# Performance work log

Hardware: AMD Instinct MI355X
Metric: run time of the kernel (lower is better)

Reference implementation:

```python
import jax, jax.numpy as jnp
import numpy as np

B, T, E, H = 4, 2048, 1024, 2048  # note: T must equal H (mask shape constraint in source)


def setup_inputs() -> dict:
    key = jax.random.key(0)
    ks = jax.random.split(key, 5)
    x = jax.random.normal(ks[0], (B, T, E), dtype=jnp.float32)
    Wq = jax.random.normal(ks[1], (E, H), dtype=jnp.float32) * 0.02
    bq = jnp.zeros((H,), dtype=jnp.float32)
    Wv = jax.random.normal(ks[2], (E, H), dtype=jnp.float32) * 0.02
    bv = jnp.zeros((H,), dtype=jnp.float32)
    return {"x": x, "Wq": Wq, "bq": bq, "Wv": Wv, "bv": bv}


def reference(x, Wq, bq, Wv, bv):
    # NOTE: original code uses q_proj for BOTH q and k (k = self.q_proj(x)),
    # so k is identical to q; k_proj params are dead. We reproduce that.
    q = x @ Wq + bq                                  # [B, T, H]
    v = x @ Wv + bv                                  # [B, T, H]
    scores = jnp.einsum('bqd,bkd->bqk', q, q)        # q @ k.mT with k == q
    scaled = scores / jnp.sqrt(jnp.float32(Wq.shape[1]))
    mask = jnp.tril(jnp.ones((scaled.shape[1], scaled.shape[2]), dtype=scaled.dtype))
    masked = scaled * mask                           # multiplicative mask (as in source)
    attn = jax.nn.softmax(masked, axis=1)            # softmax over dim=1 (query axis), as in source
    return attn @ v                                  # [B, T, H]
```

## Files before the change

### kernel.cpp

```cpp
#include <hip/hip_runtime.h>


#define B_DIM 4
#define T_DIM 2048
#define E_DIM 1024
#define H_DIM 2048

typedef __attribute__((ext_vector_type(8))) short bf16x8;
typedef __attribute__((ext_vector_type(4))) short s16x4;
typedef __attribute__((ext_vector_type(4))) float f32x4;

__device__ __forceinline__ float bf2f(short s) {
  union { float f; unsigned u; } x; x.u = ((unsigned)(unsigned short)s) << 16; return x.f;
}
__device__ __forceinline__ short f2bf(float f) {
  union { float f; unsigned u; } x; x.f = f;
  unsigned r = x.u + 0x7fff + ((x.u >> 16) & 1);
  return (short)(r >> 16);
}

__device__ __forceinline__ void gload16(const short* g, short* l) {
  __builtin_amdgcn_global_load_lds(
      (const __attribute__((address_space(1))) void*)g,
      (__attribute__((address_space(3))) void*)l, 16, 0, 0);
}

template<int MODE>
__global__ __launch_bounds__(512, 2) void gemm256(
    const short* __restrict__ Ag, const short* __restrict__ Bg,
    const float* __restrict__ bias, const float* __restrict__ bias2,
    void* __restrict__ Cg, void* __restrict__ Cg2,
    const float* __restrict__ sfx,
    int N, int K, long sA, long sB, long sC)
{
  __shared__ __align__(16) short lds[4 * 16384];

  const int t = threadIdx.x;
  const int lane = t & 63, wave = t >> 6;
  const int wm = wave >> 2, wn = wave & 3;
  const int l16 = lane & 15, kg = lane >> 4;

  int rt, ct, bz;
  if (MODE == 2) { rt = blockIdx.x; ct = blockIdx.y; bz = blockIdx.z; }
  else           { rt = blockIdx.y; ct = blockIdx.x; bz = 0; }

  const short* A  = Ag + (long)bz * sA + (long)rt * 256 * K;
  const short* Bp = Bg + (long)bz * sB + (long)ct * 256 * K;
  const int kEnd = (MODE == 2) ? (rt + 1) * 256 : K;
  const int NT = kEnd >> 5;

  const int sr = t >> 2;
  const int scg = (t & 3) ^ ((sr >> 2) & 3);
  const long a0 = (long)sr * K + scg * 8;
  const long a1 = a0 + 128L * K;

  const int swz = kg ^ ((l16 >> 2) & 3);
  const int aoff = (wm * 128 + l16) * 32 + swz * 8;
  const int boff = (wn * 64 + l16) * 32 + swz * 8;

  f32x4 acc[8][4] = {};

#pragma unroll
  for (int s = 0; s < 3; ++s) {
    short* L = &lds[s * 16384];
    const long k0 = (long)s * 32;
    gload16(A + a0 + k0, L + t * 8);
    gload16(A + a1 + k0, L + 4096 + t * 8);
    gload16(Bp + a0 + k0, L + 8192 + t * 8);
    gload16(Bp + a1 + k0, L + 12288 + t * 8);
  }
  asm volatile("s_waitcnt vmcnt(8)" ::: "memory");
  __builtin_amdgcn_s_barrier();

  for (int ts = 0; ts < NT; ++ts) {
    const short* Ab = &lds[(ts & 3) * 16384];
    const short* Bb = Ab + 8192;
    short* Ls = &lds[((ts + 3) & 3) * 16384];
    const long k3 = (long)(ts + 3) * 32;
    const bool st = (ts + 3) < NT;

    bf16x8 bfrag[4], afrag[4];
#pragma unroll
    for (int n = 0; n < 4; ++n) bfrag[n] = *(const bf16x8*)&Bb[boff + n * 512];
#pragma unroll
    for (int m = 0; m < 4; ++m) afrag[m] = *(const bf16x8*)&Ab[aoff + m * 512];
    if (st) {
      gload16(A + a0 + k3, Ls + t * 8);
      gload16(A + a1 + k3, Ls + 4096 + t * 8);
    }
    __builtin_amdgcn_s_barrier();
    __builtin_amdgcn_s_setprio(1);
#pragma unroll
    for (int m = 0; m < 4; ++m)
#pragma unroll
      for (int n = 0; n < 4; ++n)
        acc[m][n] = __builtin_amdgcn_mfma_f32_16x16x32_bf16(afrag[m], bfrag[n], acc[m][n], 0, 0, 0);
    __builtin_amdgcn_s_setprio(0);
    __builtin_amdgcn_s_barrier();
#pragma unroll
    for (int m = 0; m < 4; ++m) afrag[m] = *(const bf16x8*)&Ab[aoff + (m + 4) * 512];
    if (st) {
      gload16(Bp + a0 + k3, Ls + 8192 + t * 8);
      gload16(Bp + a1 + k3, Ls + 12288 + t * 8);
    }
    __builtin_amdgcn_s_barrier();
    __builtin_amdgcn_s_setprio(1);
#pragma unroll
    for (int m = 0; m < 4; ++m)
#pragma unroll
      for (int n = 0; n < 4; ++n)
        acc[m + 4][n] = __builtin_amdgcn_mfma_f32_16x16x32_bf16(afrag[m], bfrag[n], acc[m + 4][n], 0, 0, 0);
    __builtin_amdgcn_s_setprio(0);
    asm volatile("s_waitcnt lgkmcnt(0)" ::: "memory");
    const int w = NT - 2 - ts;
    if (w >= 2)      asm volatile("s_waitcnt vmcnt(8)" ::: "memory");
    else if (w == 1) asm volatile("s_waitcnt vmcnt(4)" ::: "memory");
    else if (w == 0) asm volatile("s_waitcnt vmcnt(0)" ::: "memory");
    __builtin_amdgcn_s_barrier();
  }

  __syncthreads();

  if (MODE == 0) {
    short* Cs = lds;
    const int Nh = N >> 1;
#pragma unroll
    for (int m = 0; m < 8; ++m)
#pragma unroll
      for (int n = 0; n < 4; ++n) {
        const int cl = wn * 64 + n * 16 + l16;
        const int colg = ct * 256 + cl;
        const float bv = (colg < Nh) ? bias[colg] : bias2[colg - Nh];
#pragma unroll
        for (int r = 0; r < 4; ++r) {
          const int rl = wm * 128 + m * 16 + kg * 4 + r;
          *(short*)((char*)Cs + (((((rl << 8) + cl) << 1)) ^ ((rl & 7) << 4))) =
              f2bf(acc[m][n][r] + bv);
        }
      }
    __syncthreads();
    short* C = ((ct * 256) < Nh) ? (short*)Cg : (short*)Cg2;
    const int rr = t >> 1, hc = (t & 1) * 128;
    const long gbase = (long)(rt * 256 + rr) * Nh + ((ct * 256) & (Nh - 1)) + hc;
#pragma unroll
    for (int j = 0; j < 16; ++j)
      *(bf16x8*)(C + gbase + j * 8) =
          *(const bf16x8*)((const char*)Cs +
              ((((rr << 8) + hc + (j << 3)) << 1) ^ ((rr & 7) << 4)));
  } else {
    float* C = (float*)Cg + (long)bz * sC;
    const float* sf = sfx + ((long)bz * 16 + 2 * rt + 1) * N;
    const int rowb = rt * 256 + wm * 128 + kg * 4;
    const int colb = ct * 256 + wn * 64 + l16;
#pragma unroll
    for (int m = 0; m < 8; ++m)
#pragma unroll
      for (int n = 0; n < 4; ++n) {
        const int col = colb + n * 16;
        const float s = sf[col];
#pragma unroll
        for (int r = 0; r < 4; ++r)
          C[(long)(rowb + m * 16 + r) * N + col] = acc[m][n][r] + s;
      }
  }
}

template<int MODE>
__global__ __launch_bounds__(256) void gemm_bt(
    const short* __restrict__ Ag, const short* __restrict__ Bg,
    const float* __restrict__ bias, const float* __restrict__ bias2,
    void* __restrict__ Cg, void* __restrict__ Cg2,
    float* __restrict__ colsum, const float* __restrict__ sfx,
    int M, int N, int K, long sA, long sB, long sC, float scale)
{
  __shared__ __align__(16) short lds[128 * 64 * 2];
  short* As = lds;
  short* Bs = lds + 128 * 64;
  __shared__ float csum[128];

  const int t = threadIdx.x;
  const int bz = blockIdx.z;

  int rt, ct;
  if (MODE == 1) {
    int idx = 135 - blockIdx.x;
    rt = (int)((sqrtf(8.0f * idx + 1.0f) - 1.0f) * 0.5f);
    while ((rt + 1) * (rt + 2) / 2 <= idx) rt++;
    while (rt * (rt + 1) / 2 > idx) rt--;
    ct = idx - rt * (rt + 1) / 2;
  } else if (MODE == 2) {
    rt = (gridDim.x - 1) - blockIdx.x;
    ct = blockIdx.y;
  } else {
    rt = blockIdx.y; ct = blockIdx.x;
  }

  const short* A = Ag + (long)bz * sA + (long)rt * 128 * K;
  const short* B = Bg + (long)bz * sB + (long)ct * 128 * K;
  const int kEnd = (MODE == 2) ? (rt + 1) * 128 : K;

  const int lane = t & 63;
  const int wave = t >> 6;
  const int wr = wave >> 1, wc = wave & 1;
  const int l16 = lane & 15, kg = lane >> 4;

  if (MODE == 1) { if (t < 128) csum[t] = (rt == ct) ? 128.0f * ct : 0.0f; }

  f32x4 acc[4][4] = {};

  for (int k0 = 0; k0 < kEnd; k0 += 64) {
    __syncthreads();
#pragma unroll
    for (int j = 0; j < 4; ++j) {
      const int e = j * 256 + t;
      const int r = e >> 3, cl = e & 7;
      const int cg = cl ^ (r & 7);
      gload16(A + (long)r * K + (k0 + cg * 8), &As[e * 8]);
      gload16(B + (long)r * K + (k0 + cg * 8), &Bs[e * 8]);
    }
    __syncthreads();
#pragma unroll
    for (int kk = 0; kk < 2; ++kk) {
      bf16x8 af[4], bfr[4];
#pragma unroll
      for (int mi = 0; mi < 4; ++mi)
        af[mi] = *(const bf16x8*)&As[(wr * 64 + mi * 16 + l16) * 64 +
                                     ((kk * 4 + kg) ^ (l16 & 7)) * 8];
#pragma unroll
      for (int ni = 0; ni < 4; ++ni)
        bfr[ni] = *(const bf16x8*)&Bs[(wc * 64 + ni * 16 + l16) * 64 +
                                      ((kk * 4 + kg) ^ (l16 & 7)) * 8];
#pragma unroll
      for (int mi = 0; mi < 4; ++mi)
#pragma unroll
        for (int ni = 0; ni < 4; ++ni)
          acc[mi][ni] = __builtin_amdgcn_mfma_f32_16x16x32_bf16(af[mi], bfr[ni], acc[mi][ni], 0, 0, 0);
    }
  }

  if (MODE == 1) {
    short* Cs = lds;
    __syncthreads();
    float ps[4] = {0.f, 0.f, 0.f, 0.f};
#pragma unroll
    for (int mi = 0; mi < 4; ++mi)
#pragma unroll
      for (int ni = 0; ni < 4; ++ni) {
        const int cl = wc * 64 + ni * 16 + l16;
        const int col = ct * 128 + cl;
#pragma unroll
        for (int r = 0; r < 4; ++r) {
          const int rl = wr * 64 + kg * 4 + mi * 16 + r;
          const int row = rt * 128 + rl;
          float e = (row >= col) ? __expf(acc[mi][ni][r] * scale) : 1.0f;
          Cs[rl * 128 + cl] = f2bf(e);
          ps[ni] += e;
        }
      }
#pragma unroll
    for (int ni = 0; ni < 4; ++ni)
      atomicAdd(&csum[wc * 64 + ni * 16 + l16], ps[ni]);
    __syncthreads();
    short* C = (short*)Cg + (long)bz * sC;
    const int rr = t >> 1, cc = (t & 1) * 64;
    const long gbase = (long)(rt * 128 + rr) * N + ct * 128 + cc;
#pragma unroll
    for (int j = 0; j < 8; ++j)
      *(bf16x8*)(C + gbase + j * 8) = *(const bf16x8*)&Cs[rr * 128 + cc + j * 8];
    if (t < 128)
      atomicAdd(&colsum[(long)bz * N + ct * 128 + t], csum[t]);
  } else if (MODE == 0) {
    short* Cs = lds;
    __syncthreads();
    const int Nh = N >> 1;
#pragma unroll
    for (int mi = 0; mi < 4; ++mi)
#pragma unroll
      for (int ni = 0; ni < 4; ++ni) {
        const int cl = wc * 64 + ni * 16 + l16;
        const int colg = ct * 128 + cl;
        const float bv = (colg < Nh) ? bias[colg] : bias2[colg - Nh];
#pragma unroll
        for (int r = 0; r < 4; ++r) {
          const int rl = wr * 64 + kg * 4 + mi * 16 + r;
          Cs[rl * 128 + cl] = f2bf(acc[mi][ni][r] + bv);
        }
      }
    __syncthreads();
    short* C = (ct * 128 < Nh) ? (short*)Cg : (short*)Cg2;
    const int colofs = (ct * 128) & (Nh - 1);
    const int rr = t >> 1, cc = (t & 1) * 64;
    const long gbase = (long)(rt * 128 + rr) * Nh + colofs + cc;
#pragma unroll
    for (int j = 0; j < 8; ++j)
      *(bf16x8*)(C + gbase + j * 8) = *(const bf16x8*)&Cs[rr * 128 + cc + j * 8];
  } else {
    const int rowb = rt * 128 + wr * 64 + kg * 4;
    const int colb = ct * 128 + wc * 64 + l16;
    float* C = (float*)Cg + (long)bz * sC;
    const float* sf = sfx + ((long)bz * 16 + rt) * N;
#pragma unroll
    for (int mi = 0; mi < 4; ++mi)
#pragma unroll
      for (int ni = 0; ni < 4; ++ni) {
        int col = colb + ni * 16;
        float s = sf[col];
#pragma unroll
        for (int r = 0; r < 4; ++r) {
          int row = rowb + mi * 16 + r;
          C[(long)row * N + col] = acc[mi][ni][r] + s;
        }
      }
  }
}

__global__ __launch_bounds__(256) void ones_fill(short* __restrict__ P)
{
  const int r = blockIdx.x, bz = blockIdx.z;
  short* p = P + (long)bz * T_DIM * T_DIM +
             (long)(2 * r) * 128 * T_DIM + (2 * r + 1) * 128;
  const int t = threadIdx.x;
  const int row = t >> 1, c0 = (t & 1) * 64;
  bf16x8 ones;
#pragma unroll
  for (int j = 0; j < 8; ++j) ones[j] = (short)0x3F80;
#pragma unroll
  for (int j = 0; j < 8; ++j)
    *(bf16x8*)(p + (long)row * T_DIM + c0 + j * 8) = ones;
}

__global__ __launch_bounds__(256) void f32_to_bf16(
    const float* __restrict__ src, short* __restrict__ dst, long n)
{
  long i = ((long)blockIdx.x * blockDim.x + threadIdx.x) * 4;
  if (i < n) {
    const float4 v = *(const float4*)(src + i);
    s16x4 o;
    o.x = f2bf(v.x); o.y = f2bf(v.y); o.z = f2bf(v.z); o.w = f2bf(v.w);
    *(s16x4*)(dst + i) = o;
  }
}

__global__ __launch_bounds__(256) void wtrans(
    const float* __restrict__ src0, const float* __restrict__ src1,
    short* __restrict__ dst)
{
  __shared__ short tile[64][65];
  const int t = threadIdx.x;
  const int c0 = blockIdx.x * 64;
  const int r0 = blockIdx.y * 64;
  const float* s = blockIdx.z ? src1 : src0;
  short* d = dst + (long)blockIdx.z * H_DIM * E_DIM;
  const int rl = t >> 4, cb = (t & 15) * 4;
#pragma unroll
  for (int i = 0; i < 4; ++i) {
    int r = rl + i * 16;
    const float4 w = *(const float4*)(s + (long)(r0 + r) * H_DIM + c0 + cb);
    tile[r][cb + 0] = f2bf(w.x); tile[r][cb + 1] = f2bf(w.y);
    tile[r][cb + 2] = f2bf(w.z); tile[r][cb + 3] = f2bf(w.w);
  }
  __syncthreads();
#pragma unroll
  for (int i = 0; i < 4; ++i) {
    int rr = rl + i * 16;
    s16x4 o;
    o.x = tile[cb + 0][rr]; o.y = tile[cb + 1][rr];
    o.z = tile[cb + 2][rr]; o.w = tile[cb + 3][rr];
    *(s16x4*)(d + (long)(c0 + rr) * E_DIM + r0 + cb) = o;
  }
}

__global__ __launch_bounds__(256) void vtrans(
    const short* __restrict__ src, short* __restrict__ dst,
    const float* __restrict__ sums)
{
  __shared__ short tile[64][65];
  const int t = threadIdx.x;
  const int c0 = blockIdx.x * 64;
  const int r0 = blockIdx.y * 64;
  const int bz = blockIdx.z;
  const short* s = src + (long)bz * T_DIM * H_DIM;
  short* d = dst + (long)bz * H_DIM * T_DIM;
  const float* su = sums + (long)bz * T_DIM;
  const int rl = t >> 4, cb = (t & 15) * 4;
#pragma unroll
  for (int i = 0; i < 4; ++i) {
    int r = rl + i * 16;
    const float rs = 1.0f / su[r0 + r];
    const s16x4 w = *(const s16x4*)(s + (long)(r0 + r) * H_DIM + c0 + cb);
    tile[r][cb + 0] = f2bf(bf2f(w.x) * rs); tile[r][cb + 1] = f2bf(bf2f(w.y) * rs);
    tile[r][cb + 2] = f2bf(bf2f(w.z) * rs); tile[r][cb + 3] = f2bf(bf2f(w.w) * rs);
  }
  __syncthreads();
#pragma unroll
  for (int i = 0; i < 4; ++i) {
    int rr = rl + i * 16;
    s16x4 o;
    o.x = tile[cb + 0][rr]; o.y = tile[cb + 1][rr];
    o.z = tile[cb + 2][rr]; o.w = tile[cb + 3][rr];
    *(s16x4*)(d + (long)(c0 + rr) * T_DIM + r0 + cb) = o;
  }
}

__global__ __launch_bounds__(256) void block_psum(
    const short* __restrict__ v, const float* __restrict__ colsum,
    float* __restrict__ psum)
{
  const int h = (blockIdx.x * 256 + threadIdx.x) * 2;
  const int j = blockIdx.y, bz = blockIdx.z;
  const short* vb = v + (long)bz * T_DIM * H_DIM;
  const float* cs = colsum + (long)bz * T_DIM;
  float s0 = 0.f, s1 = 0.f;
  const int k0 = j * 128;
  for (int k = k0; k < k0 + 128; ++k) {
    union { int i; short s[2]; } w;
    w.i = *(const int*)(vb + (long)k * H_DIM + h);
    const float rs = 1.0f / cs[k];
    s0 += bf2f(w.s[0]) * rs;
    s1 += bf2f(w.s[1]) * rs;
  }
  float* p = psum + ((long)bz * 16 + j) * H_DIM + h;
  p[0] = s0; p[1] = s1;
}

__global__ __launch_bounds__(256) void suffix_scan(
    const float* __restrict__ psum, float* __restrict__ sfx)
{
  const int h = blockIdx.x * 256 + threadIdx.x;
  const int bz = blockIdx.z;
  const long base = (long)bz * 16 * H_DIM + h;
  float suf = 0.f;
  sfx[base + 15L * H_DIM] = 0.f;
  for (int j = 15; j >= 1; --j) {
    suf += psum[base + (long)j * H_DIM];
    sfx[base + (long)(j - 1) * H_DIM] = suf;
  }
}

extern "C" void kernel_launch(void* const* d_in, const int* in_sizes, int n_in,
                              void* d_out, int out_size, void* d_ws, size_t ws_size,
                              hipStream_t stream) {
  const float* x  = (const float*)d_in[0];
  const float* Wq = (const float*)d_in[1];
  const float* bq = (const float*)d_in[2];
  const float* Wv = (const float*)d_in[3];
  const float* bv = (const float*)d_in[4];
  float* out = (float*)d_out;

  char* ws = (char*)d_ws;
  short* P      = (short*)(ws);
  short* q      = (short*)(ws + (size_t)32 * 1024 * 1024);
  short* v      = (short*)(ws + (size_t)64 * 1024 * 1024);
  float* colsum = (float*)(ws + (size_t)96 * 1024 * 1024);
  float* sfx    = (float*)(ws + (size_t)96 * 1024 * 1024 + 32 * 1024);
  short* vT = q;

  short* xb    = (short*)d_out;
  short* WqvT  = (short*)((char*)d_out + (size_t)16 * 1024 * 1024);
  float* psum  = (float*)((char*)d_out + (size_t)24 * 1024 * 1024);

  const float scale = 0.022097086912079612f;
  dim3 blk(256);

  hipMemsetAsync(colsum, 0, (size_t)B_DIM * T_DIM * 4, stream);

  f32_to_bf16<<<dim3((B_DIM * T_DIM * E_DIM) / (256 * 4)), blk, 0, stream>>>(
      x, xb, (long)B_DIM * T_DIM * E_DIM);
  wtrans<<<dim3(H_DIM / 64, E_DIM / 64, 2), blk, 0, stream>>>(Wq, Wv, WqvT);

  gemm256<0><<<dim3((2 * H_DIM) / 256, (B_DIM * T_DIM) / 256, 1), dim3(512), 0, stream>>>(
      xb, WqvT, bq, bv, q, v, nullptr, 2 * H_DIM, E_DIM, 0, 0, 0);

  gemm_bt<1><<<dim3(136, 1, B_DIM), blk, 0, stream>>>(
      q, q, nullptr, nullptr, P, nullptr, colsum, nullptr, T_DIM, T_DIM, H_DIM,
      (long)T_DIM * H_DIM, (long)T_DIM * H_DIM, (long)T_DIM * T_DIM, scale);

  ones_fill<<<dim3(8, 1, B_DIM), blk, 0, stream>>>(P);

  vtrans<<<dim3(H_DIM / 64, T_DIM / 64, B_DIM), blk, 0, stream>>>(v, vT, colsum);
  block_psum<<<dim3(H_DIM / 512, 16, B_DIM), blk, 0, stream>>>(v, colsum, psum);
  suffix_scan<<<dim3(H_DIM / 256, 1, B_DIM), blk, 0, stream>>>(psum, sfx);

  gemm256<2><<<dim3(T_DIM / 256, H_DIM / 256, B_DIM), dim3(512), 0, stream>>>(
      P, vT, nullptr, nullptr, out, nullptr, sfx, H_DIM, T_DIM,
      (long)T_DIM * T_DIM, (long)H_DIM * T_DIM, (long)T_DIM * H_DIM);
}
```

Measured before the change: 359.3 us.

## Use 64-deep K double-buffered LDS pipeline and XCD-aware block remap in gemm256

Restructures the 256x256 GEMM main loop from a 4-stage ring of 32-wide K slices to a double-buffered scheme with 64-wide K tiles, each split into two halves, using a new paired-row swizzled LDS layout. This halves loop iterations and barrier overhead per K element. For non-batched modes it also remaps linear block IDs so consecutive tiles land on the same XCD, aiming for better L2 reuse. Unused MODE 0/2 paths in the 128-tile kernel are removed. Prefetch depth drops from three stages to one, which may expose more global-load latency.

```diff
diff --git a/kernel.cpp b/kernel.cpp
--- a/kernel.cpp
+++ b/kernel.cpp
@@ -33,7 +33,7 @@
     const float* __restrict__ sfx,
     int N, int K, long sA, long sB, long sC)
 {
-  __shared__ __align__(16) short lds[4 * 16384];
+  __shared__ __align__(16) short lds[2 * 32768];
 
   const int t = threadIdx.x;
   const int lane = t & 63, wave = t >> 6;
@@ -42,81 +42,138 @@
 
   int rt, ct, bz;
   if (MODE == 2) { rt = blockIdx.x; ct = blockIdx.y; bz = blockIdx.z; }
-  else           { rt = blockIdx.y; ct = blockIdx.x; bz = 0; }
+  else {
+    int lin = blockIdx.y * gridDim.x + blockIdx.x;
+    const int cpx = (gridDim.x * gridDim.y) >> 3;
+    lin = (lin & 7) * cpx + (lin >> 3);
+    rt = lin / gridDim.x; ct = lin - rt * gridDim.x;
+    bz = 0;
+  }
 
   const short* A  = Ag + (long)bz * sA + (long)rt * 256 * K;
   const short* Bp = Bg + (long)bz * sB + (long)ct * 256 * K;
   const int kEnd = (MODE == 2) ? (rt + 1) * 256 : K;
-  const int NT = kEnd >> 5;
-
-  const int sr = t >> 2;
-  const int scg = (t & 3) ^ ((sr >> 2) & 3);
-  const long a0 = (long)sr * K + scg * 8;
-  const long a1 = a0 + 128L * K;
-
-  const int swz = kg ^ ((l16 >> 2) & 3);
-  const int aoff = (wm * 128 + l16) * 32 + swz * 8;
-  const int boff = (wn * 64 + l16) * 32 + swz * 8;
+  const int NT = kEnd >> 6;
+
+  long soff[2];
+  int dsto[2];
+#pragma unroll
+  for (int j = 0; j < 2; ++j) {
+    const int cid = j * 512 + t;
+    const int f = cid >> 3, sl = cid & 7;
+    const int c = sl ^ (f & 7);
+    soff[j] = (long)(2 * f + (c >> 2)) * K + (c & 3) * 8;
+    dsto[j] = cid * 8;
+  }
+
+  const int fl = l16 >> 1;
+  const int slot = (((l16 & 1) * 4 + kg) ^ fl) & 7;
+  const int aoff = (wm * 64 + fl) * 64 + slot * 8;
+  const int boff = (wn * 32 + fl) * 64 + slot * 8;
 
   f32x4 acc[8][4] = {};
 
-#pragma unroll
-  for (int s = 0; s < 3; ++s) {
-    short* L = &lds[s * 16384];
-    const long k0 = (long)s * 32;
-    gload16(A + a0 + k0, L + t * 8);
-    gload16(A + a1 + k0, L + 4096 + t * 8);
-    gload16(Bp + a0 + k0, L + 8192 + t * 8);
-    gload16(Bp + a1 + k0, L + 12288 + t * 8);
-  }
-  asm volatile("s_waitcnt vmcnt(8)" ::: "memory");
-  __builtin_amdgcn_s_barrier();
-
-  for (int ts = 0; ts < NT; ++ts) {
-    const short* Ab = &lds[(ts & 3) * 16384];
-    const short* Bb = Ab + 8192;
-    short* Ls = &lds[((ts + 3) & 3) * 16384];
-    const long k3 = (long)(ts + 3) * 32;
-    const bool st = (ts + 3) < NT;
-
-    bf16x8 bfrag[4], afrag[4];
-#pragma unroll
-    for (int n = 0; n < 4; ++n) bfrag[n] = *(const bf16x8*)&Bb[boff + n * 512];
-#pragma unroll
-    for (int m = 0; m < 4; ++m) afrag[m] = *(const bf16x8*)&Ab[aoff + m * 512];
-    if (st) {
-      gload16(A + a0 + k3, Ls + t * 8);
-      gload16(A + a1 + k3, Ls + 4096 + t * 8);
-    }
-    __builtin_amdgcn_s_barrier();
-    __builtin_amdgcn_s_setprio(1);
-#pragma unroll
-    for (int m = 0; m < 4; ++m)
-#pragma unroll
-      for (int n = 0; n < 4; ++n)
-        acc[m][n] = __builtin_amdgcn_mfma_f32_16x16x32_bf16(afrag[m], bfrag[n], acc[m][n], 0, 0, 0);
-    __builtin_amdgcn_s_setprio(0);
-    __builtin_amdgcn_s_barrier();
-#pragma unroll
-    for (int m = 0; m < 4; ++m) afrag[m] = *(const bf16x8*)&Ab[aoff + (m + 4) * 512];
-    if (st) {
-      gload16(Bp + a0 + k3, Ls + 8192 + t * 8);
-      gload16(Bp + a1 + k3, Ls + 12288 + t * 8);
-    }
-    __builtin_amdgcn_s_barrier();
-    __builtin_amdgcn_s_setprio(1);
-#pragma unroll
-    for (int m = 0; m < 4; ++m)
-#pragma unroll
-      for (int n = 0; n < 4; ++n)
-        acc[m + 4][n] = __builtin_amdgcn_mfma_f32_16x16x32_bf16(afrag[m], bfrag[n], acc[m + 4][n], 0, 0, 0);
-    __builtin_amdgcn_s_setprio(0);
-    asm volatile("s_waitcnt lgkmcnt(0)" ::: "memory");
-    const int w = NT - 2 - ts;
-    if (w >= 2)      asm volatile("s_waitcnt vmcnt(8)" ::: "memory");
-    else if (w == 1) asm volatile("s_waitcnt vmcnt(4)" ::: "memory");
-    else if (w == 0) asm volatile("s_waitcnt vmcnt(0)" ::: "memory");
-    __builtin_amdgcn_s_barrier();
+  {
+    short* S = lds;
+#pragma unroll
+    for (int kh = 0; kh < 2; ++kh)
+#pragma unroll
+      for (int j = 0; j < 2; ++j) {
+        gload16(A  + soff[j] + kh * 32, &S[kh * 8192 + dsto[j]]);
+        gload16(Bp + soff[j] + kh * 32, &S[16384 + kh * 8192 + dsto[j]]);
+      }
+  }
+  asm volatile("s_waitcnt vmcnt(4)" ::: "memory");
+  asm volatile("s_barrier" ::: "memory");
+
+  for (int T = 0; T < NT; ++T) {
+    const short* Abase = lds + (T & 1) * 32768;
+    short* S = lds + ((T + 1) & 1) * 32768;
+    const long kIss = (long)(T + 1) * 64;
+    const bool st = (T + 1) < NT;
+    bf16x8 bfr[4], af[4];
+
+    {
+      const short* Ab = Abase;
+      const short* Bb = Abase + 16384;
+#pragma unroll
+      for (int n = 0; n < 4; ++n) bfr[n] = *(const bf16x8*)&Bb[boff + n * 512];
+#pragma unroll
+      for (int m = 0; m < 4; ++m) af[m] = *(const bf16x8*)&Ab[aoff + m * 512];
+      if (st) {
+        gload16(A + soff[0] + kIss, &S[dsto[0]]);
+        gload16(A + soff[1] + kIss, &S[dsto[1]]);
+      }
+      asm volatile("s_barrier" ::: "memory");
+      __builtin_amdgcn_s_setprio(1);
+#pragma unroll
+      for (int m = 0; m < 4; ++m)
+#pragma unroll
+        for (int n = 0; n < 4; ++n)
+          acc[m][n] = __builtin_amdgcn_mfma_f32_16x16x32_bf16(af[m], bfr[n], acc[m][n], 0, 0, 0);
+      __builtin_amdgcn_s_setprio(0);
+      asm volatile("s_barrier" ::: "memory");
+    }
+    {
+      const short* Ab = Abase;
+#pragma unroll
+      for (int m = 0; m < 4; ++m) af[m] = *(const bf16x8*)&Ab[aoff + (m + 4) * 512];
+      if (st) {
+        gload16(Bp + soff[0] + kIss, &S[16384 + dsto[0]]);
+        gload16(Bp + soff[1] + kIss, &S[16384 + dsto[1]]);
+      }
+      asm volatile("s_barrier" ::: "memory");
+      __builtin_amdgcn_s_setprio(1);
+#pragma unroll
+      for (int m = 0; m < 4; ++m)
+#pragma unroll
+        for (int n = 0; n < 4; ++n)
+          acc[m + 4][n] = __builtin_amdgcn_mfma_f32_16x16x32_bf16(af[m], bfr[n], acc[m + 4][n], 0, 0, 0);
+      __builtin_amdgcn_s_setprio(0);
+      if (T == NT - 1) asm volatile("s_waitcnt vmcnt(0)" ::: "memory");
+      else             asm volatile("s_waitcnt vmcnt(4)" ::: "memory");
+      asm volatile("s_barrier" ::: "memory");
+    }
+    {
+      const short* Ab = Abase + 8192;
+      const short* Bb = Abase + 16384 + 8192;
+#pragma unroll
+      for (int n = 0; n < 4; ++n) bfr[n] = *(const bf16x8*)&Bb[boff + n * 512];
+#pragma unroll
+      for (int m = 0; m < 4; ++m) af[m] = *(const bf16x8*)&Ab[aoff + m * 512];
+      if (st) {
+        gload16(A + soff[0] + kIss + 32, &S[8192 + dsto[0]]);
+        gload16(A + soff[1] + kIss + 32, &S[8192 + dsto[1]]);
+      }
+      asm volatile("s_barrier" ::: "memory");
+      __builtin_amdgcn_s_setprio(1);
+#pragma unroll
+      for (int m = 0; m < 4; ++m)
+#pragma unroll
+        for (int n = 0; n < 4; ++n)
+          acc[m][n] = __builtin_amdgcn_mfma_f32_16x16x32_bf16(af[m], bfr[n], acc[m][n], 0, 0, 0);
+      __builtin_amdgcn_s_setprio(0);
+      asm volatile("s_barrier" ::: "memory");
+    }
+    {
+      const short* Ab = Abase + 8192;
+#pragma unroll
+      for (int m = 0; m < 4; ++m) af[m] = *(const bf16x8*)&Ab[aoff + (m + 4) * 512];
+      if (st) {
+        gload16(Bp + soff[0] + kIss + 32, &S[16384 + 8192 + dsto[0]]);
+        gload16(Bp + soff[1] + kIss + 32, &S[16384 + 8192 + dsto[1]]);
+      }
+      asm volatile("s_barrier" ::: "memory");
+      __builtin_amdgcn_s_setprio(1);
+#pragma unroll
+      for (int m = 0; m < 4; ++m)
+#pragma unroll
+        for (int n = 0; n < 4; ++n)
+          acc[m + 4][n] = __builtin_amdgcn_mfma_f32_16x16x32_bf16(af[m], bfr[n], acc[m + 4][n], 0, 0, 0);
+      __builtin_amdgcn_s_setprio(0);
+      if (st) asm volatile("s_waitcnt vmcnt(4)" ::: "memory");
+      asm volatile("s_barrier" ::: "memory");
+    }
   }
 
   __syncthreads();
@@ -188,16 +245,13 @@
     while ((rt + 1) * (rt + 2) / 2 <= idx) rt++;
     while (rt * (rt + 1) / 2 > idx) rt--;
     ct = idx - rt * (rt + 1) / 2;
-  } else if (MODE == 2) {
-    rt = (gridDim.x - 1) - blockIdx.x;
-    ct = blockIdx.y;
   } else {
     rt = blockIdx.y; ct = blockIdx.x;
   }
 
   const short* A = Ag + (long)bz * sA + (long)rt * 128 * K;
   const short* B = Bg + (long)bz * sB + (long)ct * 128 * K;
-  const int kEnd = (MODE == 2) ? (rt + 1) * 128 : K;
+  const int kEnd = K;
 
   const int lane = t & 63;
   const int wave = t >> 6;
@@ -269,48 +323,6 @@
       *(bf16x8*)(C + gbase + j * 8) = *(const bf16x8*)&Cs[rr * 128 + cc + j * 8];
     if (t < 128)
       atomicAdd(&colsum[(long)bz * N + ct * 128 + t], csum[t]);
-  } else if (MODE == 0) {
-    short* Cs = lds;
-    __syncthreads();
-    const int Nh = N >> 1;
-#pragma unroll
-    for (int mi = 0; mi < 4; ++mi)
-#pragma unroll
-      for (int ni = 0; ni < 4; ++ni) {
-        const int cl = wc * 64 + ni * 16 + l16;
-        const int colg = ct * 128 + cl;
-        const float bv = (colg < Nh) ? bias[colg] : bias2[colg - Nh];
-#pragma unroll
-        for (int r = 0; r < 4; ++r) {
-          const int rl = wr * 64 + kg * 4 + mi * 16 + r;
-          Cs[rl * 128 + cl] = f2bf(acc[mi][ni][r] + bv);
-        }
-      }
-    __syncthreads();
-    short* C = (ct * 128 < Nh) ? (short*)Cg : (short*)Cg2;
-    const int colofs = (ct * 128) & (Nh - 1);
-    const int rr = t >> 1, cc = (t & 1) * 64;
-    const long gbase = (long)(rt * 128 + rr) * Nh + colofs + cc;
-#pragma unroll
-    for (int j = 0; j < 8; ++j)
-      *(bf16x8*)(C + gbase + j * 8) = *(const bf16x8*)&Cs[rr * 128 + cc + j * 8];
-  } else {
-    const int rowb = rt * 128 + wr * 64 + kg * 4;
-    const int colb = ct * 128 + wc * 64 + l16;
-    float* C = (float*)Cg + (long)bz * sC;
-    const float* sf = sfx + ((long)bz * 16 + rt) * N;
-#pragma unroll
-    for (int mi = 0; mi < 4; ++mi)
-#pragma unroll
-      for (int ni = 0; ni < 4; ++ni) {
-        int col = colb + ni * 16;
-        float s = sf[col];
-#pragma unroll
-        for (int r = 0; r < 4; ++r) {
-          int row = rowb + mi * 16 + r;
-          C[(long)row * N + col] = acc[mi][ni][r] + s;
-        }
-      }
   }
 }
 
```

After: 359.0 us. No clear change (-0.1%).
